# Optimization experiments

Hardware: AMD Instinct MI355X
Metric: run time of the kernel (lower is better)

The kernel has to match this reference:

```python
import jax, jax.numpy as jnp
import numpy as np

STRIDE = 1
PADDING = 1
DILATION = 1


def _conv_one(xi, wi):
    # xi: [C_in, H, W], wi: [C_out, C_in, ks, ks]
    out = jax.lax.conv_general_dilated(
        xi[None],  # [1, C_in, H, W]
        wi,
        window_strides=(STRIDE, STRIDE),
        padding=[(PADDING, PADDING), (PADDING, PADDING)],
        rhs_dilation=(DILATION, DILATION),
        dimension_numbers=("NCHW", "OIHW", "NCHW"),
    )
    return out[0]  # [C_out, H', W']


def setup_inputs() -> dict:
    key = jax.random.key(0)
    k1, k2, k3 = jax.random.split(key, 3)
    B, C_in, C_out, H, W, ks = 32, 32, 32, 256, 256, 3
    x = jax.random.normal(k1, (B, C_in, H, W), dtype=jnp.float32)
    weight = jax.random.normal(k2, (B, C_out, C_in, ks, ks), dtype=jnp.float32)
    bias = jax.random.normal(k3, (B, C_out), dtype=jnp.float32)
    return {"x": x, "weight": weight, "bias": bias}


def reference(x, weight, bias):
    # Per-sample conv: sample i of x convolved with weight[i].
    out = jax.vmap(_conv_one)(x, weight)  # [B, C_out, H', W']
    out = out + bias[:, :, None, None]
    return out
```

## Files before the change

### kernel.cpp

```cpp
#include <hip/hip_runtime.h>


#define BB 32
#define CI 32
#define CO 32
#define HH 256
#define WW 256

typedef unsigned int uint;
using short8  = __attribute__((ext_vector_type(8))) short;
using float4v = __attribute__((ext_vector_type(4))) float;

__device__ inline unsigned short f2bf(float f) {
    union { float f; uint u; } c; c.f = f;
    uint r = c.u + 0x7fffu + ((c.u >> 16) & 1u);
    return (unsigned short)(r >> 16);
}

__device__ inline uint pk2bf(float lo, float hi) {
    uint r;
    asm("v_cvt_pk_bf16_f32 %0, %1, %2" : "=v"(r) : "v"(lo), "v"(hi));
    return r;
}

__global__ __launch_bounds__(256)
void wconv_kernel(const float* __restrict__ wgt,
                  unsigned short* __restrict__ wb) {
    const int i = blockIdx.x * 256 + threadIdx.x;
    const int bc  = i / 288;
    const int rem = i - bc * 288;
    const int ci  = rem / 9;
    const int tap = rem - ci * 9;
    wb[(bc * 9 + tap) * CI + ci] = f2bf(wgt[i]);
}

#define TH 16
#define TW 32
#define XR (TH + 2)
#define XC 40

__device__ inline int swz_us(int pix, int q) {
    return pix * CI + (((q ^ (pix >> 1)) & 3) << 3);
}

__global__ __launch_bounds__(512)
void conv_fused_kernel(const float* __restrict__ x,
                       const unsigned short* __restrict__ wb,
                       const float* __restrict__ bias,
                       float* __restrict__ out) {
    __shared__ __align__(16) unsigned short xs[XR * XC * CI];

    const int tw = blockIdx.x;
    const int th = blockIdx.y;
    const int b  = blockIdx.z;
    const int t  = threadIdx.x;
    const int h0 = th * TH, w0 = tw * TW;

    const int wv  = t >> 6;
    const int l   = t & 63;
    const int lp  = l & 15;
    const int lq  = l >> 4;

    const unsigned short* wbb = wb + (size_t)(b * CO) * 9 * CI;
    short8 W0[9], W1[9];
    #pragma unroll
    for (int tp = 0; tp < 9; ++tp) {
        W0[tp] = *(const short8*)(wbb + ((lp)      * 9 + tp) * CI + lq * 8);
        W1[tp] = *(const short8*)(wbb + ((16 + lp) * 9 + tp) * CI + lq * 8);
    }

    const float* xb = x + (size_t)b * CI * HH * WW;
    for (int i = t; i < XR * 10 * 4; i += 512) {
        const int qd  = i / 10;
        const int f   = i - qd * 10;
        const int ciq = qd & 3;
        const int rr  = qd >> 2;
        const int h   = h0 - 1 + rr;
        const int c4  = w0 - 4 + 4 * f;
        float4v v[8];
        if (h >= 0 && h < HH && c4 >= 0 && c4 <= WW - 4) {
            const float* p0 = xb + (size_t)(ciq * 8) * HH * WW
                                 + (size_t)h * WW + c4;
            #pragma unroll
            for (int j = 0; j < 8; ++j)
                v[j] = *(const float4v*)(p0 + (size_t)j * HH * WW);
        } else {
            #pragma unroll
            for (int j = 0; j < 8; ++j) v[j] = {0.f, 0.f, 0.f, 0.f};
        }
        #pragma unroll
        for (int e = 0; e < 4; ++e) {
            const int p = rr * XC + 4 * f + e;
            uint4 pk;
            pk.x = pk2bf(v[0][e], v[1][e]);
            pk.y = pk2bf(v[2][e], v[3][e]);
            pk.z = pk2bf(v[4][e], v[5][e]);
            pk.w = pk2bf(v[6][e], v[7][e]);
            *(uint4*)(&xs[swz_us(p, ciq)]) = pk;
        }
    }
    __syncthreads();

    float4v acc0[4], acc1[4];
    #pragma unroll
    for (int g = 0; g < 4; ++g) {
        acc0[g] = {0.f, 0.f, 0.f, 0.f};
        acc1[g] = {0.f, 0.f, 0.f, 0.f};
    }

    #pragma unroll
    for (int g = 0; g < 4; ++g) {
        const int gg = wv * 4 + g;
        const int r  = gg >> 1;
        const int c0 = (gg & 1) * 16;
        #pragma unroll
        for (int kh = 0; kh < 3; ++kh) {
            #pragma unroll
            for (int kw = 0; kw < 3; ++kw) {
                const int p = (r + kh) * XC + (c0 + lp + kw + 3);
                short8 Pf = *(const short8*)(&xs[swz_us(p, lq)]);
                acc0[g] = __builtin_amdgcn_mfma_f32_16x16x32_bf16(
                    Pf, W0[kh * 3 + kw], acc0[g], 0, 0, 0);
                acc1[g] = __builtin_amdgcn_mfma_f32_16x16x32_bf16(
                    Pf, W1[kh * 3 + kw], acc1[g], 0, 0, 0);
            }
        }
    }

    const float bv0 = bias[b * CO + lp];
    const float bv1 = bias[b * CO + 16 + lp];

    #pragma unroll
    for (int g = 0; g < 4; ++g) {
        const int gg = wv * 4 + g;
        const int r  = gg >> 1;
        const int c0 = (gg & 1) * 16;
        const int h  = h0 + r;
        const int wb4 = w0 + c0 + lq * 4;
        float4v o0 = acc0[g] + bv0;
        float4v o1 = acc1[g] + bv1;
        *(float4v*)(&out[(((size_t)(b * CO + lp)) * HH + h) * WW + wb4]) = o0;
        *(float4v*)(&out[(((size_t)(b * CO + 16 + lp)) * HH + h) * WW + wb4]) = o1;
    }
}

#define FHT 16
#define FXR (FHT + 2)
#define LROW 264

__global__ __launch_bounds__(256)
void conv3x3_fallback(const float* __restrict__ x,
                      const float* __restrict__ wgt,
                      const float* __restrict__ bias,
                      float* __restrict__ out) {
    __shared__ float xs[FXR * LROW];
    __shared__ float wsh[CI * 9];
    const int co = blockIdx.x;
    const int ht = blockIdx.y;
    const int b  = blockIdx.z;
    const int tid = threadIdx.x;
    const int h0 = ht * FHT;
    for (int i = tid; i < CI * 9; i += 256)
        wsh[i] = wgt[((size_t)(b * CO + co) * CI) * 9 + i];
    for (int i = tid; i < FXR * 8; i += 256) {
        int row = i >> 3; int c = i & 7;
        int col = (c < 4) ? c : (256 + c);
        xs[row * LROW + col] = 0.0f;
    }
    const int wg = tid & 63, rp = tid >> 6;
    const int w0 = wg * 4, r0 = rp * 4;
    float acc[4][4];
    #pragma unroll
    for (int d = 0; d < 4; ++d)
        #pragma unroll
        for (int j = 0; j < 4; ++j) acc[d][j] = 0.0f;
    const float* xb = x + (size_t)(b * CI) * HH * WW;
    for (int ci = 0; ci < CI; ++ci) {
        __syncthreads();
        const float* xsrc = xb + (size_t)ci * HH * WW;
        for (int i = tid; i < FXR * 64; i += 256) {
            int row = i >> 6; int cq = i & 63;
            int gh = h0 - 1 + row;
            float4 v = make_float4(0.f, 0.f, 0.f, 0.f);
            if (gh >= 0 && gh < HH)
                v = *(const float4*)(xsrc + (size_t)gh * WW + cq * 4);
            *(float4*)(&xs[row * LROW + 4 + cq * 4]) = v;
        }
        __syncthreads();
        float wk[9];
        #pragma unroll
        for (int k = 0; k < 9; ++k) wk[k] = wsh[ci * 9 + k];
        #pragma unroll
        for (int xr = 0; xr < 6; ++xr) {
            const float* rowp = &xs[(r0 + xr) * LROW + w0];
            float xv[12];
            #pragma unroll
            for (int q = 0; q < 3; ++q) {
                float4 v = *(const float4*)(rowp + 4 * q);
                xv[4*q+0] = v.x; xv[4*q+1] = v.y; xv[4*q+2] = v.z; xv[4*q+3] = v.w;
            }
            #pragma unroll
            for (int dr = 0; dr < 4; ++dr) {
                const int kh = xr - dr;
                if (kh < 0 || kh > 2) continue;
                #pragma unroll
                for (int kw = 0; kw < 3; ++kw) {
                    const float wvv = wk[kh * 3 + kw];
                    #pragma unroll
                    for (int j = 0; j < 4; ++j)
                        acc[dr][j] += xv[j + kw + 3] * wvv;
                }
            }
        }
    }
    const float bv = bias[b * CO + co];
    float* ob = out + ((size_t)(b * CO + co) * HH + (h0 + r0)) * WW + w0;
    #pragma unroll
    for (int dr = 0; dr < 4; ++dr) {
        float4 o;
        o.x = acc[dr][0] + bv; o.y = acc[dr][1] + bv;
        o.z = acc[dr][2] + bv; o.w = acc[dr][3] + bv;
        *(float4*)(ob + (size_t)dr * WW) = o;
    }
}

extern "C" void kernel_launch(void* const* d_in, const int* in_sizes, int n_in,
                              void* d_out, int out_size, void* d_ws, size_t ws_size,
                              hipStream_t stream) {
    const float* x    = (const float*)d_in[0];
    const float* wgt  = (const float*)d_in[1];
    const float* bias = (const float*)d_in[2];
    float* out        = (float*)d_out;

    const size_t wb_bytes = (size_t)BB * CO * 9 * CI * sizeof(unsigned short);
    if (ws_size >= wb_bytes) {
        unsigned short* wbp = (unsigned short*)d_ws;
        hipLaunchKernelGGL(wconv_kernel, dim3((BB * CO * CI * 9) / 256), dim3(256),
                           0, stream, wgt, wbp);
        hipLaunchKernelGGL(conv_fused_kernel, dim3(WW / TW, HH / TH, BB), dim3(512),
                           0, stream, x, wbp, bias, out);
    } else {
        hipLaunchKernelGGL(conv3x3_fallback, dim3(CO, HH / FHT, BB), dim3(256),
                           0, stream, x, wgt, bias, out);
    }
}
```

Baseline: 493.8 us.

## Make conv blocks persistent over row strips with double-buffered LDS prefetch

Each block now walks a strip of eight 8-row tiles instead of one 16-row tile. The next tile's global loads are issued into registers before the MFMA work on the current tile and are committed to a second LDS buffer afterwards. This hides global load latency behind compute and amortises the per-block weight register loads. In exchange, halo overhead per output row rises because tiles are shorter, the grid is smaller, and more registers are needed to hold the prefetch.

```diff
diff --git a/kernel.cpp b/kernel.cpp
--- a/kernel.cpp
+++ b/kernel.cpp
@@ -34,33 +34,82 @@
     wb[(bc * 9 + tap) * CI + ci] = f2bf(wgt[i]);
 }
 
-#define TH 16
+#define TH 8
 #define TW 32
 #define XR (TH + 2)
 #define XC 40
+#define NT 8
+#define NITEM (XR * 10 * 4)
+#define BUFE (XR * XC * CI)
 
 __device__ inline int swz_us(int pix, int q) {
     return pix * CI + (((q ^ (pix >> 1)) & 3) << 3);
 }
 
-__global__ __launch_bounds__(512)
-void conv_fused_kernel(const float* __restrict__ x,
+struct Pre { float4v v[8]; };
+
+__device__ inline void issue_item(const float* __restrict__ xb, int item,
+                                  int hb, int w0, Pre& P) {
+    const int qd  = item / 10;
+    const int f   = item - qd * 10;
+    const int ciq = qd & 3;
+    const int rr  = qd >> 2;
+    const int h   = hb - 1 + rr;
+    const int c4  = w0 - 4 + 4 * f;
+    if (h >= 0 && h < HH && c4 >= 0 && c4 <= WW - 4) {
+        const float* p0 = xb + (size_t)(ciq * 8) * HH * WW
+                             + (size_t)h * WW + c4;
+        #pragma unroll
+        for (int j = 0; j < 8; ++j)
+            P.v[j] = *(const float4v*)(p0 + (size_t)j * HH * WW);
+    } else {
+        #pragma unroll
+        for (int j = 0; j < 8; ++j) P.v[j] = {0.f, 0.f, 0.f, 0.f};
+    }
+}
+
+__device__ inline void commit_item(unsigned short* __restrict__ buf, int item,
+                                   const Pre& P) {
+    const int qd  = item / 10;
+    const int f   = item - qd * 10;
+    const int ciq = qd & 3;
+    const int rr  = qd >> 2;
+    #pragma unroll
+    for (int e = 0; e < 4; ++e) {
+        const int p = rr * XC + 4 * f + e;
+        uint4 pk;
+        pk.x = pk2bf(P.v[0][e], P.v[1][e]);
+        pk.y = pk2bf(P.v[2][e], P.v[3][e]);
+        pk.z = pk2bf(P.v[4][e], P.v[5][e]);
+        pk.w = pk2bf(P.v[6][e], P.v[7][e]);
+        *(uint4*)(&buf[swz_us(p, ciq)]) = pk;
+    }
+}
+
+__global__ __launch_bounds__(512, 2)
+void conv_strip_kernel(const float* __restrict__ x,
                        const unsigned short* __restrict__ wb,
                        const float* __restrict__ bias,
                        float* __restrict__ out) {
-    __shared__ __align__(16) unsigned short xs[XR * XC * CI];
-
-    const int tw = blockIdx.x;
-    const int th = blockIdx.y;
-    const int b  = blockIdx.z;
-    const int t  = threadIdx.x;
-    const int h0 = th * TH, w0 = tw * TW;
+    __shared__ __align__(16) unsigned short xs[2][BUFE];
+
+    const int tw  = blockIdx.x;
+    const int th4 = blockIdx.y;
+    const int b   = blockIdx.z;
+    const int t   = threadIdx.x;
+    const int w0  = tw * TW;
+    const int hb0 = th4 * (TH * NT);
 
     const int wv  = t >> 6;
     const int l   = t & 63;
     const int lp  = l & 15;
     const int lq  = l >> 4;
 
+    const float* xb = x + (size_t)b * CI * HH * WW;
+
+    Pre P0;
+    if (t < NITEM) issue_item(xb, t, hb0, w0, P0);
+
     const unsigned short* wbb = wb + (size_t)(b * CO) * 9 * CI;
     short8 W0[9], W1[9];
     #pragma unroll
@@ -68,79 +117,62 @@
         W0[tp] = *(const short8*)(wbb + ((lp)      * 9 + tp) * CI + lq * 8);
         W1[tp] = *(const short8*)(wbb + ((16 + lp) * 9 + tp) * CI + lq * 8);
     }
-
-    const float* xb = x + (size_t)b * CI * HH * WW;
-    for (int i = t; i < XR * 10 * 4; i += 512) {
-        const int qd  = i / 10;
-        const int f   = i - qd * 10;
-        const int ciq = qd & 3;
-        const int rr  = qd >> 2;
-        const int h   = h0 - 1 + rr;
-        const int c4  = w0 - 4 + 4 * f;
-        float4v v[8];
-        if (h >= 0 && h < HH && c4 >= 0 && c4 <= WW - 4) {
-            const float* p0 = xb + (size_t)(ciq * 8) * HH * WW
-                                 + (size_t)h * WW + c4;
-            #pragma unroll
-            for (int j = 0; j < 8; ++j)
-                v[j] = *(const float4v*)(p0 + (size_t)j * HH * WW);
-        } else {
-            #pragma unroll
-            for (int j = 0; j < 8; ++j) v[j] = {0.f, 0.f, 0.f, 0.f};
-        }
-        #pragma unroll
-        for (int e = 0; e < 4; ++e) {
-            const int p = rr * XC + 4 * f + e;
-            uint4 pk;
-            pk.x = pk2bf(v[0][e], v[1][e]);
-            pk.y = pk2bf(v[2][e], v[3][e]);
-            pk.z = pk2bf(v[4][e], v[5][e]);
-            pk.w = pk2bf(v[6][e], v[7][e]);
-            *(uint4*)(&xs[swz_us(p, ciq)]) = pk;
-        }
-    }
-    __syncthreads();
-
-    float4v acc0[4], acc1[4];
-    #pragma unroll
-    for (int g = 0; g < 4; ++g) {
-        acc0[g] = {0.f, 0.f, 0.f, 0.f};
-        acc1[g] = {0.f, 0.f, 0.f, 0.f};
-    }
-
-    #pragma unroll
-    for (int g = 0; g < 4; ++g) {
-        const int gg = wv * 4 + g;
-        const int r  = gg >> 1;
-        const int c0 = (gg & 1) * 16;
-        #pragma unroll
-        for (int kh = 0; kh < 3; ++kh) {
-            #pragma unroll
-            for (int kw = 0; kw < 3; ++kw) {
-                const int p = (r + kh) * XC + (c0 + lp + kw + 3);
-                short8 Pf = *(const short8*)(&xs[swz_us(p, lq)]);
-                acc0[g] = __builtin_amdgcn_mfma_f32_16x16x32_bf16(
-                    Pf, W0[kh * 3 + kw], acc0[g], 0, 0, 0);
-                acc1[g] = __builtin_amdgcn_mfma_f32_16x16x32_bf16(
-                    Pf, W1[kh * 3 + kw], acc1[g], 0, 0, 0);
-            }
-        }
-    }
-
     const float bv0 = bias[b * CO + lp];
     const float bv1 = bias[b * CO + 16 + lp];
 
-    #pragma unroll
-    for (int g = 0; g < 4; ++g) {
-        const int gg = wv * 4 + g;
-        const int r  = gg >> 1;
-        const int c0 = (gg & 1) * 16;
-        const int h  = h0 + r;
-        const int wb4 = w0 + c0 + lq * 4;
-        float4v o0 = acc0[g] + bv0;
-        float4v o1 = acc1[g] + bv1;
-        *(float4v*)(&out[(((size_t)(b * CO + lp)) * HH + h) * WW + wb4]) = o0;
-        *(float4v*)(&out[(((size_t)(b * CO + 16 + lp)) * HH + h) * WW + wb4]) = o1;
+    if (t < NITEM) commit_item(&xs[0][0], t, P0);
+    __syncthreads();
+
+    for (int tt = 0; tt < NT; ++tt) {
+        unsigned short* cur = &xs[tt & 1][0];
+        unsigned short* nxt = &xs[(tt & 1) ^ 1][0];
+        const int hb = hb0 + tt * TH;
+
+        if (tt < NT - 1 && t < NITEM)
+            issue_item(xb, t, hb + TH, w0, P0);
+
+        float4v acc0[2], acc1[2];
+        #pragma unroll
+        for (int g = 0; g < 2; ++g) {
+            acc0[g] = {0.f, 0.f, 0.f, 0.f};
+            acc1[g] = {0.f, 0.f, 0.f, 0.f};
+        }
+        #pragma unroll
+        for (int g = 0; g < 2; ++g) {
+            const int gg = wv * 2 + g;
+            const int r  = gg >> 1;
+            const int c0 = (gg & 1) * 16;
+            #pragma unroll
+            for (int kh = 0; kh < 3; ++kh) {
+                #pragma unroll
+                for (int kw = 0; kw < 3; ++kw) {
+                    const int p = (r + kh) * XC + (c0 + lp + kw + 3);
+                    short8 Pf = *(const short8*)(&cur[swz_us(p, lq)]);
+                    acc0[g] = __builtin_amdgcn_mfma_f32_16x16x32_bf16(
+                        Pf, W0[kh * 3 + kw], acc0[g], 0, 0, 0);
+                    acc1[g] = __builtin_amdgcn_mfma_f32_16x16x32_bf16(
+                        Pf, W1[kh * 3 + kw], acc1[g], 0, 0, 0);
+                }
+            }
+        }
+
+        if (tt < NT - 1) {
+            if (t < NITEM) commit_item(nxt, t, P0);
+            __syncthreads();
+        }
+
+        #pragma unroll
+        for (int g = 0; g < 2; ++g) {
+            const int gg = wv * 2 + g;
+            const int r  = gg >> 1;
+            const int c0 = (gg & 1) * 16;
+            const int h  = hb + r;
+            const int wb4 = w0 + c0 + lq * 4;
+            float4v o0 = acc0[g] + bv0;
+            float4v o1 = acc1[g] + bv1;
+            *(float4v*)(&out[(((size_t)(b * CO + lp)) * HH + h) * WW + wb4]) = o0;
+            *(float4v*)(&out[(((size_t)(b * CO + 16 + lp)) * HH + h) * WW + wb4]) = o1;
+        }
     }
 }
 
@@ -237,7 +269,8 @@
         unsigned short* wbp = (unsigned short*)d_ws;
         hipLaunchKernelGGL(wconv_kernel, dim3((BB * CO * CI * 9) / 256), dim3(256),
                            0, stream, wgt, wbp);
-        hipLaunchKernelGGL(conv_fused_kernel, dim3(WW / TW, HH / TH, BB), dim3(512),
+        hipLaunchKernelGGL(conv_strip_kernel,
+                           dim3(WW / TW, HH / (TH * NT), BB), dim3(512),
                            0, stream, x, wbp, bias, out);
     } else {
         hipLaunchKernelGGL(conv3x3_fallback, dim3(CO, HH / FHT, BB), dim3(256),
```

After: 526.1 us. 1.07x slower.
